# Kernel tuning notes

Hardware: AMD Instinct MI355X
Metric: run time of the kernel (lower is better)

## Reference

```python
import jax, jax.numpy as jnp
import numpy as np

EPS_BN = 1e-5

def _l2n(v, axis):
    return v / jnp.maximum(jnp.linalg.norm(v, axis=axis, keepdims=True), 1e-12)

def _bn_relu(x, g, b):
    # x: [B, C, K]; BatchNorm2d training-mode stats over (B, K) per channel, then ReLU
    m = x.mean(axis=(0, 2), keepdims=True)
    v = x.var(axis=(0, 2), keepdims=True)
    return jax.nn.relu(g[None, :, None] * (x - m) * jax.lax.rsqrt(v + EPS_BN) + b[None, :, None])

def _conv_bn_relu(x, W, g, b):
    # 1x1 conv (no bias) == channel matmul
    return _bn_relu(jnp.einsum('oi,bik->bok', W, x), g, b)

def _graphnet(x, anchor, sigma_p):
    # NetVLAD-style soft assignment; vectorized over clusters (no [B,K,N,C] intermediate)
    B, C, H, W = x.shape
    N = H * W
    sig = jax.nn.sigmoid(sigma_p)                              # [K, C]
    xf = x.reshape(B, C, N).transpose(0, 2, 1)                 # [B, N, C]
    inv_s2 = 1.0 / (sig * sig)                                 # [K, C]
    q = (jnp.einsum('bnc,kc->bnk', xf * xf, inv_s2)
         - 2.0 * jnp.einsum('bnc,kc->bnk', xf, anchor * inv_s2)
         + jnp.sum(anchor * anchor * inv_s2, axis=-1))         # [B, N, K]
    assign = jax.nn.softmax(-0.5 * q.transpose(0, 2, 1), axis=1)  # [B, K, N], softmax over clusters
    s = assign.sum(axis=-1)                                    # [B, K]
    wx = jnp.einsum('bkn,bnc->bkc', assign, xf)                # [B, K, C]
    nodes = (wx - s[..., None] * anchor[None]) / sig[None] / (s[..., None] + 1e-9)
    nodes = _l2n(nodes, 2)
    flat = _l2n(nodes.reshape(B, -1), 1)
    # faithful to torch: flat view as (B, C, K) is a pure reshape of [B, K, C] data
    return flat.reshape(B, C, anchor.shape[0]), assign

def _cascade_gcn(x, W1, W2):
    # loop=2 cascaded GCN: adj = softmax(x^T x), out = (adj @ (x^T W))^T
    for Wg in (W1, W2):
        adj = jax.nn.softmax(jnp.einsum('bik,bil->bkl', x, x), axis=2)   # [B, K, K]
        sup = jnp.einsum('bik,io->bko', x, Wg)                           # [B, K, C]
        x = jnp.einsum('bkl,blo->bok', adj, sup)                         # [B, C, K]
    return jax.nn.relu(x)

def _mutual(edge, r1, r2, assign, g1, g2, cw, cg, cb):
    # cross-graph correlation + cascade GCN + project back to pixels
    a = jax.nn.softmax(jnp.einsum('bik,bil->bkl', edge, r1), axis=-1)    # [B, K, K]
    m = jnp.einsum('bkl,bcl->bck', a, r2)                                # [B, C, K]
    edge = _cascade_gcn(edge + m, g1, g2)
    ex = jnp.einsum('bck,bkn->bcn', edge, assign)                        # [B, C, N]
    return _conv_bn_relu(ex, cw, cg, cb)


def setup_inputs() -> dict:
    key = jax.random.key(0)
    B, C, H, W, K = 16, 256, 64, 64, 8
    ks = jax.random.split(key, 40)
    sc = 1.0 / np.sqrt(C)
    d = {
        'rgb':   jax.random.normal(ks[0], (B, C, H, W), jnp.float32),
        't':     jax.random.normal(ks[1], (B, C, H, W), jnp.float32),
        'edger': jax.random.normal(ks[2], (B, C, H, W), jnp.float32),
        'edget': jax.random.normal(ks[3], (B, C, H, W), jnp.float32),
        'pred_w': jax.random.normal(ks[4], (1, C), jnp.float32) * sc,
        'pred_b': jax.random.normal(ks[5], (1,), jnp.float32) * 0.1,
        'rgb_anchor': jax.random.uniform(ks[6], (K, C), jnp.float32),
        'rgb_sigma':  jax.random.uniform(ks[7], (K, C), jnp.float32),
        't_anchor':   jax.random.uniform(ks[8], (K, C), jnp.float32),
        't_sigma':    jax.random.uniform(ks[9], (K, C), jnp.float32),
    }
    i = 10
    for name in ['rgb_c1', 'rgb_c2', 't_c1', 't_c2', 't2r_conv', 'r2t_conv']:
        d[name + '_w'] = jax.random.normal(ks[i], (C, C), jnp.float32) * sc; i += 1
        d[name + '_g'] = jax.random.uniform(ks[i], (C,), jnp.float32); i += 1
        d[name + '_b'] = jnp.zeros((C,), jnp.float32)
    for name in ['t2r_g1', 't2r_g2', 'r2t_g1', 'r2t_g2']:
        d[name + '_w'] = jax.random.normal(ks[i], (C, C), jnp.float32) * sc; i += 1
    return d


def reference(rgb, t, edger, edget, pred_w, pred_b,
              rgb_anchor, rgb_sigma, t_anchor, t_sigma,
              rgb_c1_w, rgb_c1_g, rgb_c1_b, rgb_c2_w, rgb_c2_g, rgb_c2_b,
              t_c1_w, t_c1_g, t_c1_b, t_c2_w, t_c2_g, t_c2_b,
              t2r_conv_w, t2r_conv_g, t2r_conv_b,
              r2t_conv_w, r2t_conv_g, r2t_conv_b,
              t2r_g1_w, t2r_g2_w, r2t_g1_w, r2t_g2_w):
    # edge-gated features
    edge_r = jnp.einsum('oi,bihw->bohw', pred_w, edger) + pred_b.reshape(1, -1, 1, 1)
    rgb_x = jax.nn.sigmoid(edge_r) * rgb
    edge_t = jnp.einsum('oi,bihw->bohw', pred_w, edget) + pred_b.reshape(1, -1, 1, 1)
    t_x = jax.nn.sigmoid(edge_t) * t
    # graph projection
    rgb_graph, rgb_assign = _graphnet(rgb_x, rgb_anchor, rgb_sigma)
    t_graph, t_assign = _graphnet(t_x, t_anchor, t_sigma)
    rgb_g1 = _conv_bn_relu(rgb_graph, rgb_c1_w, rgb_c1_g, rgb_c1_b)
    rgb_g2 = _conv_bn_relu(rgb_graph, rgb_c2_w, rgb_c2_g, rgb_c2_b)
    t_g1 = _conv_bn_relu(t_graph, t_c1_w, t_c1_g, t_c1_b)
    t_g2 = _conv_bn_relu(t_graph, t_c2_w, t_c2_g, t_c2_b)
    # mutual graph interaction
    n_rgb = _mutual(rgb_graph, t_g1, t_g2, rgb_assign, t2r_g1_w, t2r_g2_w,
                    t2r_conv_w, t2r_conv_g, t2r_conv_b)
    rgb_x = rgb_x + n_rgb.reshape(rgb_x.shape)
    n_t = _mutual(t_graph, rgb_g1, rgb_g2, t_assign, r2t_g1_w, r2t_g2_w,
                  r2t_conv_w, r2t_conv_g, r2t_conv_b)
    t_x = t_x + n_t.reshape(t_x.shape)
    return (rgb_x, t_x)
```

## Files before the change

kernel.cpp:

```cpp
#include <hip/hip_runtime.h>
#include <math.h>

#define BB 16
#define CC 256
#define NN 4096
#define KK 8

#define OFF_S      ((size_t)0)
#define OFF_WX     ((size_t)256)
#define OFF_G      ((size_t)65792)
#define OFF_CS     ((size_t)67840)
#define OFF_MS     ((size_t)69888)
#define OFF_CK     ((size_t)70912)
#define ACC_FLOATS ((size_t)70928)
#define OFF_ASSIGN ((size_t)70928)
#define OFF_GRAPH  ((size_t)1119504)
#define OFF_CLP    ((size_t)1185040)
#define OFF_WT     ((size_t)1193232)
#define OFF_Y      ((size_t)1586448)
#define OFF_CE     ((size_t)1717520)
#define WS_FLOATS  ((size_t)1783056)

__global__ __launch_bounds__(256) void k0_prep(
    const float* __restrict__ w0, const float* __restrict__ w1,
    const float* __restrict__ w2, const float* __restrict__ w3,
    const float* __restrict__ w4, const float* __restrict__ w5,
    const float* __restrict__ anch_r, const float* __restrict__ sig_r,
    const float* __restrict__ anch_t, const float* __restrict__ sig_t,
    float* __restrict__ ws)
{
    int bid = blockIdx.x, tid = threadIdx.x;
    if (bid < 1536) {
        int widx = bid >> 8;
        int e = ((bid & 255) << 8) + tid;
        int o = e >> 8, i = e & 255;
        const float* W = widx == 0 ? w0 : widx == 1 ? w1 : widx == 2 ? w2 :
                         widx == 3 ? w3 : widx == 4 ? w4 : w5;
        ws[OFF_WT + (size_t)widx * 65536 + (size_t)i * 256 + o] = W[o * 256 + i];
    } else {
        int pid = ((bid - 1536) << 8) + tid;
        int M = pid >> 11, j = pid & 2047;
        const float* sg = M ? sig_t : sig_r;
        const float* an = M ? anch_t : anch_r;
        float s = 1.f / (1.f + expf(-sg[j]));
        float is2 = 1.f / (s * s);
        float a = an[j];
        float2* c2 = (float2*)(ws + OFF_CLP);
        c2[(size_t)M * 2048 + j] = make_float2(is2, -2.f * a * is2);
        atomicAdd(&ws[OFF_CK + (size_t)M * 8 + (j >> 8)], a * a * is2);
    }
}

__global__ __launch_bounds__(256) void k1_gate_assign(
    const float* __restrict__ rgb, const float* __restrict__ t,
    const float* __restrict__ edger, const float* __restrict__ edget,
    const float* __restrict__ pred_w, const float* __restrict__ pred_b,
    float* __restrict__ out, float* __restrict__ ws)
{
    int tile = blockIdx.x;
    int b    = blockIdx.y;
    int M    = blockIdx.z;
    int tid  = threadIdx.x;
    int tx = tid & 63, ty = tid >> 6;
    int n0 = tile * 64;

    const float* X = M ? t : rgb;
    const float* E = M ? edget : edger;

    __shared__ _Float16 xs[CC][66];
    __shared__ float2 pr_s[2048];
    __shared__ float qp[KK][4][64];
    __shared__ float gatep[4][64];
    __shared__ float gate[64];
    __shared__ float asg[KK][64];
    __shared__ float cks[KK];

    const float2* pr = (const float2*)(ws + OFF_CLP) + (size_t)M * 2048;
    for (int i = tid; i < 2048; i += 256) pr_s[i] = pr[i];
    if (tid < KK) cks[tid] = ws[OFF_CK + (size_t)M * 8 + tid];

    const float* Eb = E + ((size_t)b * CC) * NN + n0 + tx;
    float acc = 0.f;
    for (int c = ty * 64; c < ty * 64 + 64; ++c)
        acc += pred_w[c] * Eb[(size_t)c * NN];
    gatep[ty][tx] = acc;
    __syncthreads();
    if (tid < 64) {
        float g = gatep[0][tx] + gatep[1][tx] + gatep[2][tx] + gatep[3][tx] + pred_b[0];
        gate[tx] = 1.f / (1.f + expf(-g));
    }
    __syncthreads();

    const float* Xb = X + ((size_t)b * CC) * NN + n0 + tx;
    float* Ob = out + (((size_t)M * BB + b) * CC) * NN + n0 + tx;
    float gt = gate[tx];
    float qk[KK];
#pragma unroll
    for (int k = 0; k < KK; ++k) qk[k] = 0.f;
    for (int c = ty * 64; c < ty * 64 + 64; ++c) {
        float x = gt * Xb[(size_t)c * NN];
        Ob[(size_t)c * NN] = x;
        xs[c][tx] = (_Float16)x;
        float xx = x * x;
#pragma unroll
        for (int k = 0; k < KK; ++k) {
            float2 p = pr_s[k * 256 + c];
            qk[k] += xx * p.x + x * p.y;
        }
    }
#pragma unroll
    for (int k = 0; k < KK; ++k) qp[k][ty][tx] = qk[k];
    __syncthreads();

    float* assign_g = ws + OFF_ASSIGN + (((size_t)M * BB + b) * KK) * NN;
    if (tid < 64) {
        float q[KK], mx = -1e30f;
#pragma unroll
        for (int k = 0; k < KK; ++k) {
            q[k] = -0.5f * (qp[k][0][tx] + qp[k][1][tx] + qp[k][2][tx] + qp[k][3][tx] + cks[k]);
            mx = fmaxf(mx, q[k]);
        }
        float sm = 0.f;
#pragma unroll
        for (int k = 0; k < KK; ++k) { q[k] = expf(q[k] - mx); sm += q[k]; }
        float inv = 1.f / sm;
#pragma unroll
        for (int k = 0; k < KK; ++k) {
            float a = q[k] * inv;
            asg[k][tx] = a;
            assign_g[(size_t)k * NN + n0 + tx] = a;
        }
    }
    __syncthreads();

    {
        int c = tid;
        float a0[KK];
#pragma unroll
        for (int k = 0; k < KK; ++k) a0[k] = 0.f;
        for (int j = 0; j < 64; ++j) {
            float xv = (float)xs[c][j];
#pragma unroll
            for (int k = 0; k < KK; ++k) a0[k] += asg[k][j] * xv;
        }
        float* wx_g = ws + OFF_WX + ((size_t)M * BB + b) * KK * CC;
#pragma unroll
        for (int k = 0; k < KK; ++k)
            atomicAdd(&wx_g[k * CC + c], a0[k]);
    }
    if (tid < 64) {
        int k1 = tid >> 3, k2 = tid & 7;
        float g = 0.f;
        for (int j = 0; j < 64; ++j) g += asg[k1][j] * asg[k2][j];
        atomicAdd(&ws[OFF_G + ((size_t)M * BB + b) * 64 + tid], g);
    } else if (tid < 72) {
        int k = tid - 64;
        float sv = 0.f;
        for (int j = 0; j < 64; ++j) sv += asg[k][j];
        atomicAdd(&ws[OFF_S + ((size_t)M * BB + b) * KK + k], sv);
    }
}

__global__ __launch_bounds__(256) void k2_nodes(
    const float* __restrict__ anch_r, const float* __restrict__ sig_r,
    const float* __restrict__ anch_t, const float* __restrict__ sig_t,
    float* __restrict__ ws)
{
    int b = blockIdx.x & 15, M = blockIdx.x >> 4;
    int c = threadIdx.x;
    const float* an = M ? anch_t : anch_r;
    const float* sg = M ? sig_t : sig_r;
    const float* wx = ws + OFF_WX + ((size_t)M * BB + b) * KK * CC;
    const float* sp = ws + OFF_S + ((size_t)M * BB + b) * KK;
    float* gout = ws + OFF_GRAPH + ((size_t)M * BB + b) * 2048;

    __shared__ float nod[KK][CC];
    __shared__ float nrm[KK];
    __shared__ float gp[CC];
    __shared__ float gnrm;

    float node[KK];
#pragma unroll
    for (int k = 0; k < KK; ++k) {
        float s = sp[k];
        float sig = 1.f / (1.f + expf(-sg[k * CC + c]));
        float v = (wx[k * CC + c] - s * an[k * CC + c]) / sig / (s + 1e-9f);
        node[k] = v;
        nod[k][c] = v;
    }
    __syncthreads();
    if (c < KK) {
        float ss = 0.f;
        for (int i = 0; i < CC; ++i) ss += nod[c][i] * nod[c][i];
        nrm[c] = fmaxf(sqrtf(ss), 1e-12f);
    }
    __syncthreads();
    float gs = 0.f;
#pragma unroll
    for (int k = 0; k < KK; ++k) { node[k] /= nrm[k]; gs += node[k] * node[k]; }
    gp[c] = gs;
    __syncthreads();
    if (c == 0) {
        float ss = 0.f;
        for (int i = 0; i < CC; ++i) ss += gp[i];
        gnrm = fmaxf(sqrtf(ss), 1e-12f);
    }
    __syncthreads();
    float inv = 1.f / gnrm;
#pragma unroll
    for (int k = 0; k < KK; ++k)
        gout[k * CC + c] = node[k] * inv;
}

__global__ __launch_bounds__(256) void k3_conv(float* __restrict__ ws)
{
    int conv = blockIdx.x >> 4, b = blockIdx.x & 15;
    int o = threadIdx.x;
    int M = conv >> 1;
    const float* gsrc = ws + OFF_GRAPH + ((size_t)M * BB + b) * 2048;
    const float* wt = ws + OFF_WT + (size_t)conv * 65536;
    __shared__ float gsh[2048];
    for (int i = o; i < 2048; i += 256) gsh[i] = gsrc[i];
    __syncthreads();
    float acc[KK];
#pragma unroll
    for (int k = 0; k < KK; ++k) acc[k] = 0.f;
    for (int i = 0; i < CC; ++i) {
        float w = wt[(size_t)i * 256 + o];
#pragma unroll
        for (int k = 0; k < KK; ++k) acc[k] += w * gsh[i * 8 + k];
    }
    float* y = ws + OFF_Y + ((size_t)conv * BB + b) * 2048;
    float s1 = 0.f, s2 = 0.f;
#pragma unroll
    for (int k = 0; k < KK; ++k) { y[o * 8 + k] = acc[k]; s1 += acc[k]; s2 += acc[k] * acc[k]; }
    atomicAdd(&ws[OFF_CS + (size_t)conv * 512 + o], s1);
    atomicAdd(&ws[OFF_CS + (size_t)conv * 512 + 256 + o], s2);
}

__device__ __forceinline__ void gcn_layer(const float* __restrict__ Wg,
                                          float* xin, float* xout, float* am,
                                          float* sup, int o, bool do_relu)
{
    if (o < 64) {
        int k = o >> 3, l = o & 7;
        float s = 0.f;
        for (int i = 0; i < CC; ++i) s += xin[i * 9 + k] * xin[i * 9 + l];
        am[k * 9 + l] = s;
    }
    __syncthreads();
    if (o < 8) {
        float mx = -1e30f;
#pragma unroll
        for (int l = 0; l < 8; ++l) mx = fmaxf(mx, am[o * 9 + l]);
        float e[8], sm = 0.f;
#pragma unroll
        for (int l = 0; l < 8; ++l) { e[l] = expf(am[o * 9 + l] - mx); sm += e[l]; }
        float inv = 1.f / sm;
#pragma unroll
        for (int l = 0; l < 8; ++l) am[o * 9 + l] = e[l] * inv;
    }
    float sa[8];
#pragma unroll
    for (int k = 0; k < 8; ++k) sa[k] = 0.f;
    for (int i = 0; i < CC; ++i) {
        float w = Wg[(size_t)i * 256 + o];
#pragma unroll
        for (int k = 0; k < 8; ++k) sa[k] += xin[i * 9 + k] * w;
    }
#pragma unroll
    for (int k = 0; k < 8; ++k) sup[k * 256 + o] = sa[k];
    __syncthreads();
#pragma unroll
    for (int k = 0; k < 8; ++k) {
        float v = 0.f;
#pragma unroll
        for (int l = 0; l < 8; ++l) v += am[k * 9 + l] * sup[l * 256 + o];
        xout[o * 9 + k] = do_relu ? fmaxf(v, 0.f) : v;
    }
    __syncthreads();
}

__global__ __launch_bounds__(256) void k4_mutual(
    const float* __restrict__ rc1g, const float* __restrict__ rc1b,
    const float* __restrict__ rc2g, const float* __restrict__ rc2b,
    const float* __restrict__ tc1g, const float* __restrict__ tc1b,
    const float* __restrict__ tc2g, const float* __restrict__ tc2b,
    const float* __restrict__ t2rg1, const float* __restrict__ t2rg2,
    const float* __restrict__ r2tg1, const float* __restrict__ r2tg2,
    float* __restrict__ ws)
{
    int D = blockIdx.x >> 4, b = blockIdx.x & 15;
    int o = threadIdx.x;
    int M = D;
    int convR1 = D ? 0 : 2;
    int convR2 = D ? 1 : 3;
    const float* g1p = D ? rc1g : tc1g;  const float* b1p = D ? rc1b : tc1b;
    const float* g2p = D ? rc2g : tc2g;  const float* b2p = D ? rc2b : tc2b;
    const float* gcn1 = D ? r2tg1 : t2rg1;
    const float* gcn2 = D ? r2tg2 : t2rg2;
    const float* cwT = ws + OFF_WT + (size_t)(4 + D) * 65536;

    __shared__ float edge_s[CC * 9];
    __shared__ float r1_s[CC * 9];
    __shared__ float r2_s[CC * 9];
    __shared__ float x0[CC * 9];
    __shared__ float x1[CC * 9];
    __shared__ float sup[KK * CC];
    __shared__ float am[KK * 9];
    __shared__ float sS[KK];
    __shared__ float gS[64];

    if (o < 8)  sS[o] = ws[OFF_S + ((size_t)M * BB + b) * 8 + o];
    if (o < 64) gS[o] = ws[OFF_G + ((size_t)M * BB + b) * 64 + o];

    const float* egr = ws + OFF_GRAPH + ((size_t)M * BB + b) * 2048;
    const float* y1 = ws + OFF_Y + ((size_t)convR1 * BB + b) * 2048;
    const float* y2 = ws + OFF_Y + ((size_t)convR2 * BB + b) * 2048;
    float m1 = ws[OFF_CS + (size_t)convR1 * 512 + o] * (1.f / 128.f);
    float q1 = ws[OFF_CS + (size_t)convR1 * 512 + 256 + o] * (1.f / 128.f);
    float al1 = g1p[o] * rsqrtf(q1 - m1 * m1 + 1e-5f);
    float be1 = b1p[o] - m1 * al1;
    float m2 = ws[OFF_CS + (size_t)convR2 * 512 + o] * (1.f / 128.f);
    float q2 = ws[OFF_CS + (size_t)convR2 * 512 + 256 + o] * (1.f / 128.f);
    float al2 = g2p[o] * rsqrtf(q2 - m2 * m2 + 1e-5f);
    float be2 = b2p[o] - m2 * al2;
#pragma unroll
    for (int k = 0; k < 8; ++k) {
        edge_s[o * 9 + k] = egr[o * 8 + k];
        r1_s[o * 9 + k] = fmaxf(al1 * y1[o * 8 + k] + be1, 0.f);
        r2_s[o * 9 + k] = fmaxf(al2 * y2[o * 8 + k] + be2, 0.f);
    }
    __syncthreads();

    if (o < 64) {
        int k = o >> 3, l = o & 7;
        float s = 0.f;
        for (int i = 0; i < CC; ++i) s += edge_s[i * 9 + k] * r1_s[i * 9 + l];
        am[k * 9 + l] = s;
    }
    __syncthreads();
    if (o < 8) {
        float mx = -1e30f;
#pragma unroll
        for (int l = 0; l < 8; ++l) mx = fmaxf(mx, am[o * 9 + l]);
        float e[8], sm = 0.f;
#pragma unroll
        for (int l = 0; l < 8; ++l) { e[l] = expf(am[o * 9 + l] - mx); sm += e[l]; }
        float inv = 1.f / sm;
#pragma unroll
        for (int l = 0; l < 8; ++l) am[o * 9 + l] = e[l] * inv;
    }
    __syncthreads();

#pragma unroll
    for (int k = 0; k < 8; ++k) {
        float mm = 0.f;
#pragma unroll
        for (int l = 0; l < 8; ++l) mm += am[k * 9 + l] * r2_s[o * 9 + l];
        x0[o * 9 + k] = edge_s[o * 9 + k] + mm;
    }
    __syncthreads();

    gcn_layer(gcn1, x0, x1, am, sup, o, false);
    gcn_layer(gcn2, x1, x0, am, sup, o, true);

    float ac[8];
#pragma unroll
    for (int k = 0; k < 8; ++k) ac[k] = 0.f;
    for (int i = 0; i < CC; ++i) {
        float w = cwT[(size_t)i * 256 + o];
#pragma unroll
        for (int k = 0; k < 8; ++k) ac[k] += w * x0[i * 9 + k];
    }
    float* ce = ws + OFF_CE + ((size_t)D * BB + b) * 2048;
    float smv = 0.f, sqv = 0.f;
#pragma unroll
    for (int k = 0; k < 8; ++k) {
        ce[o * 8 + k] = ac[k];
        smv += ac[k] * sS[k];
#pragma unroll
        for (int l = 0; l < 8; ++l) sqv += ac[k] * ac[l] * gS[k * 8 + l];
    }
    atomicAdd(&ws[OFF_MS + (size_t)D * 512 + o], smv);
    atomicAdd(&ws[OFF_MS + (size_t)D * 512 + 256 + o], sqv);
}

__global__ __launch_bounds__(256) void k6_final(
    const float* __restrict__ t2rg, const float* __restrict__ t2rb,
    const float* __restrict__ r2tg, const float* __restrict__ r2tb,
    float* __restrict__ out, const float* __restrict__ ws)
{
    int chunk = blockIdx.x >> 2, cq = blockIdx.x & 3;
    int b = blockIdx.y, D = blockIdx.z;
    int tid = threadIdx.x;
    int n = chunk * 256 + tid;

    const float* assign_g = ws + OFF_ASSIGN + (((size_t)D * BB + b) * KK) * NN;
    float areg[KK];
#pragma unroll
    for (int k = 0; k < KK; ++k) areg[k] = assign_g[(size_t)k * NN + n];

    __shared__ float ce_s[64 * 8];
    __shared__ float al_s[64], be_s[64];
    const float* ce = ws + OFF_CE + ((size_t)D * BB + b) * 2048 + (size_t)cq * 512;
    for (int i = tid; i < 512; i += 256) ce_s[i] = ce[i];
    if (tid < 64) {
        int o = cq * 64 + tid;
        float m = ws[OFF_MS + (size_t)D * 512 + o] * (1.f / 65536.f);
        float q = ws[OFF_MS + (size_t)D * 512 + 256 + o] * (1.f / 65536.f);
        float var = q - m * m;
        const float* g = D ? r2tg : t2rg;
        const float* bb = D ? r2tb : t2rb;
        float al = g[o] * rsqrtf(var + 1e-5f);
        al_s[tid] = al;
        be_s[tid] = bb[o] - m * al;
    }
    __syncthreads();

    float* ob = out + (((size_t)D * BB + b) * CC + (size_t)cq * 64) * NN + n;
    for (int cc = 0; cc < 64; ++cc) {
        float y = 0.f;
#pragma unroll
        for (int k = 0; k < KK; ++k) y += ce_s[cc * 8 + k] * areg[k];
        float v = fmaxf(al_s[cc] * y + be_s[cc], 0.f);
        ob[(size_t)cc * NN] += v;
    }
}

extern "C" void kernel_launch(void* const* d_in, const int* in_sizes, int n_in,
                              void* d_out, int out_size, void* d_ws, size_t ws_size,
                              hipStream_t stream) {
    (void)in_sizes; (void)n_in; (void)out_size; (void)ws_size;
    const float* rgb    = (const float*)d_in[0];
    const float* t      = (const float*)d_in[1];
    const float* edger  = (const float*)d_in[2];
    const float* edget  = (const float*)d_in[3];
    const float* pred_w = (const float*)d_in[4];
    const float* pred_b = (const float*)d_in[5];
    const float* anch_r = (const float*)d_in[6];
    const float* sig_r  = (const float*)d_in[7];
    const float* anch_t = (const float*)d_in[8];
    const float* sig_t  = (const float*)d_in[9];
    const float* rc1w = (const float*)d_in[10];
    const float* rc1g = (const float*)d_in[11];
    const float* rc1b = (const float*)d_in[12];
    const float* rc2w = (const float*)d_in[13];
    const float* rc2g = (const float*)d_in[14];
    const float* rc2b = (const float*)d_in[15];
    const float* tc1w = (const float*)d_in[16];
    const float* tc1g = (const float*)d_in[17];
    const float* tc1b = (const float*)d_in[18];
    const float* tc2w = (const float*)d_in[19];
    const float* tc2g = (const float*)d_in[20];
    const float* tc2b = (const float*)d_in[21];
    const float* t2rcw = (const float*)d_in[22];
    const float* t2rcg = (const float*)d_in[23];
    const float* t2rcb = (const float*)d_in[24];
    const float* r2tcw = (const float*)d_in[25];
    const float* r2tcg = (const float*)d_in[26];
    const float* r2tcb = (const float*)d_in[27];
    const float* t2rg1 = (const float*)d_in[28];
    const float* t2rg2 = (const float*)d_in[29];
    const float* r2tg1 = (const float*)d_in[30];
    const float* r2tg2 = (const float*)d_in[31];

    float* out = (float*)d_out;
    float* ws = (float*)d_ws;

    hipMemsetAsync(ws, 0, ACC_FLOATS * sizeof(float), stream);
    k0_prep<<<1552, 256, 0, stream>>>(rc1w, rc2w, tc1w, tc2w, t2rcw, r2tcw,
                                      anch_r, sig_r, anch_t, sig_t, ws);
    k1_gate_assign<<<dim3(64, 16, 2), 256, 0, stream>>>(rgb, t, edger, edget,
                                                        pred_w, pred_b, out, ws);
    k2_nodes<<<32, 256, 0, stream>>>(anch_r, sig_r, anch_t, sig_t, ws);
    k3_conv<<<64, 256, 0, stream>>>(ws);
    k4_mutual<<<32, 256, 0, stream>>>(rc1g, rc1b, rc2g, rc2b, tc1g, tc1b, tc2g, tc2b,
                                      t2rg1, t2rg2, r2tg1, r2tg2, ws);
    k6_final<<<dim3(64, 16, 2), 256, 0, stream>>>(t2rcg, t2rcb, r2tcg, r2tcb, out, ws);
}
```

Before: 594.5 us.

## Recompute gated features in final kernel instead of writing then re-reading output

The gate-assign kernel no longer writes the full gated feature map to the output. It stores only the per-pixel gate value in channel 0 of the output slot. The final kernel reads that gate and the original input, recomputes gate*x and adds the graph term in a single write, removing one full-tensor write and one read-modify-write pass. The prep kernel's cluster parameters are re-laid out as [c][k] so they can be read with float4 global loads instead of being staged in shared memory, and the final kernel uses 512-thread blocks covering all 256 channels. The cost is re-reading the input tensor in the final kernel.

```diff
diff --git a/kernel.cpp b/kernel.cpp
--- a/kernel.cpp
+++ b/kernel.cpp
@@ -40,14 +40,15 @@
     } else {
         int pid = ((bid - 1536) << 8) + tid;
         int M = pid >> 11, j = pid & 2047;
+        int k = j >> 8, c = j & 255;
         const float* sg = M ? sig_t : sig_r;
         const float* an = M ? anch_t : anch_r;
         float s = 1.f / (1.f + expf(-sg[j]));
         float is2 = 1.f / (s * s);
         float a = an[j];
         float2* c2 = (float2*)(ws + OFF_CLP);
-        c2[(size_t)M * 2048 + j] = make_float2(is2, -2.f * a * is2);
-        atomicAdd(&ws[OFF_CK + (size_t)M * 8 + (j >> 8)], a * a * is2);
+        c2[(size_t)M * 2048 + (size_t)c * 8 + k] = make_float2(is2, -2.f * a * is2);
+        atomicAdd(&ws[OFF_CK + (size_t)M * 8 + k], a * a * is2);
     }
 }
 
@@ -68,45 +69,48 @@
     const float* E = M ? edget : edger;
 
     __shared__ _Float16 xs[CC][66];
-    __shared__ float2 pr_s[2048];
     __shared__ float qp[KK][4][64];
     __shared__ float gatep[4][64];
-    __shared__ float gate[64];
+    __shared__ float gate_s[64];
     __shared__ float asg[KK][64];
     __shared__ float cks[KK];
 
-    const float2* pr = (const float2*)(ws + OFF_CLP) + (size_t)M * 2048;
-    for (int i = tid; i < 2048; i += 256) pr_s[i] = pr[i];
     if (tid < KK) cks[tid] = ws[OFF_CK + (size_t)M * 8 + tid];
 
     const float* Eb = E + ((size_t)b * CC) * NN + n0 + tx;
     float acc = 0.f;
+#pragma unroll 4
     for (int c = ty * 64; c < ty * 64 + 64; ++c)
         acc += pred_w[c] * Eb[(size_t)c * NN];
     gatep[ty][tx] = acc;
     __syncthreads();
     if (tid < 64) {
         float g = gatep[0][tx] + gatep[1][tx] + gatep[2][tx] + gatep[3][tx] + pred_b[0];
-        gate[tx] = 1.f / (1.f + expf(-g));
+        float sg = 1.f / (1.f + expf(-g));
+        gate_s[tx] = sg;
+        out[(((size_t)M * BB + b) * CC) * NN + n0 + tx] = sg;
     }
     __syncthreads();
 
     const float* Xb = X + ((size_t)b * CC) * NN + n0 + tx;
-    float* Ob = out + (((size_t)M * BB + b) * CC) * NN + n0 + tx;
-    float gt = gate[tx];
+    const float4* prq = (const float4*)(ws + OFF_CLP) + (size_t)M * 1024;
+    float gt = gate_s[tx];
     float qk[KK];
 #pragma unroll
     for (int k = 0; k < KK; ++k) qk[k] = 0.f;
+#pragma unroll 2
     for (int c = ty * 64; c < ty * 64 + 64; ++c) {
         float x = gt * Xb[(size_t)c * NN];
-        Ob[(size_t)c * NN] = x;
         xs[c][tx] = (_Float16)x;
         float xx = x * x;
-#pragma unroll
-        for (int k = 0; k < KK; ++k) {
-            float2 p = pr_s[k * 256 + c];
-            qk[k] += xx * p.x + x * p.y;
-        }
+        float4 p0 = prq[c * 4 + 0];
+        float4 p1 = prq[c * 4 + 1];
+        float4 p2 = prq[c * 4 + 2];
+        float4 p3 = prq[c * 4 + 3];
+        qk[0] += xx * p0.x + x * p0.y;  qk[1] += xx * p0.z + x * p0.w;
+        qk[2] += xx * p1.x + x * p1.y;  qk[3] += xx * p1.z + x * p1.w;
+        qk[4] += xx * p2.x + x * p2.y;  qk[5] += xx * p2.z + x * p2.w;
+        qk[6] += xx * p3.x + x * p3.y;  qk[7] += xx * p3.z + x * p3.w;
     }
 #pragma unroll
     for (int k = 0; k < KK; ++k) qp[k][ty][tx] = qk[k];
@@ -138,6 +142,7 @@
         float a0[KK];
 #pragma unroll
         for (int k = 0; k < KK; ++k) a0[k] = 0.f;
+#pragma unroll 4
         for (int j = 0; j < 64; ++j) {
             float xv = (float)xs[c][j];
 #pragma unroll
@@ -386,45 +391,56 @@
     atomicAdd(&ws[OFF_MS + (size_t)D * 512 + 256 + o], sqv);
 }
 
-__global__ __launch_bounds__(256) void k6_final(
+__global__ __launch_bounds__(512) void k6_final(
+    const float* __restrict__ rgb, const float* __restrict__ t,
     const float* __restrict__ t2rg, const float* __restrict__ t2rb,
     const float* __restrict__ r2tg, const float* __restrict__ r2tb,
     float* __restrict__ out, const float* __restrict__ ws)
 {
-    int chunk = blockIdx.x >> 2, cq = blockIdx.x & 3;
+    int chunk = blockIdx.x;
     int b = blockIdx.y, D = blockIdx.z;
     int tid = threadIdx.x;
-    int n = chunk * 256 + tid;
+    int tn = tid & 255, th = tid >> 8;
+    int n = chunk * 256 + tn;
+
+    const float* X = D ? t : rgb;
+    float* obase = out + (((size_t)D * BB + b) * CC) * NN;
+
+    float gt = obase[n];
 
     const float* assign_g = ws + OFF_ASSIGN + (((size_t)D * BB + b) * KK) * NN;
-    float areg[KK];
-#pragma unroll
-    for (int k = 0; k < KK; ++k) areg[k] = assign_g[(size_t)k * NN + n];
-
-    __shared__ float ce_s[64 * 8];
-    __shared__ float al_s[64], be_s[64];
-    const float* ce = ws + OFF_CE + ((size_t)D * BB + b) * 2048 + (size_t)cq * 512;
-    for (int i = tid; i < 512; i += 256) ce_s[i] = ce[i];
-    if (tid < 64) {
-        int o = cq * 64 + tid;
+    float a0 = assign_g[0 * NN + n], a1 = assign_g[1 * NN + n];
+    float a2 = assign_g[2 * NN + n], a3 = assign_g[3 * NN + n];
+    float a4 = assign_g[4 * NN + n], a5 = assign_g[5 * NN + n];
+    float a6 = assign_g[6 * NN + n], a7 = assign_g[7 * NN + n];
+
+    __shared__ __align__(16) float ce_s[2048];
+    __shared__ float al_s[256], be_s[256];
+    const float* ce = ws + OFF_CE + ((size_t)D * BB + b) * 2048;
+    for (int i = tid; i < 2048; i += 512) ce_s[i] = ce[i];
+    if (tid < 256) {
+        int o = tid;
         float m = ws[OFF_MS + (size_t)D * 512 + o] * (1.f / 65536.f);
         float q = ws[OFF_MS + (size_t)D * 512 + 256 + o] * (1.f / 65536.f);
-        float var = q - m * m;
         const float* g = D ? r2tg : t2rg;
         const float* bb = D ? r2tb : t2rb;
-        float al = g[o] * rsqrtf(var + 1e-5f);
-        al_s[tid] = al;
-        be_s[tid] = bb[o] - m * al;
-    }
-    __syncthreads();
-
-    float* ob = out + (((size_t)D * BB + b) * CC + (size_t)cq * 64) * NN + n;
-    for (int cc = 0; cc < 64; ++cc) {
-        float y = 0.f;
-#pragma unroll
-        for (int k = 0; k < KK; ++k) y += ce_s[cc * 8 + k] * areg[k];
-        float v = fmaxf(al_s[cc] * y + be_s[cc], 0.f);
-        ob[(size_t)cc * NN] += v;
+        float al = g[o] * rsqrtf(q - m * m + 1e-5f);
+        al_s[o] = al;
+        be_s[o] = bb[o] - m * al;
+    }
+    __syncthreads();
+
+    const float* Xb = X + ((size_t)b * CC) * NN + n;
+    const float4* ce4 = (const float4*)ce_s;
+#pragma unroll 4
+    for (int i = 0; i < 128; ++i) {
+        int c = th * 128 + i;
+        float4 ca = ce4[2 * c];
+        float4 cb = ce4[2 * c + 1];
+        float y = ca.x * a0 + ca.y * a1 + ca.z * a2 + ca.w * a3
+                + cb.x * a4 + cb.y * a5 + cb.z * a6 + cb.w * a7;
+        float v = fmaxf(al_s[c] * y + be_s[c], 0.f);
+        obase[(size_t)c * NN + n] = gt * Xb[(size_t)c * NN] + v;
     }
 }
 
@@ -477,5 +493,6 @@
     k3_conv<<<64, 256, 0, stream>>>(ws);
     k4_mutual<<<32, 256, 0, stream>>>(rc1g, rc1b, rc2g, rc2b, tc1g, tc1b, tc2g, tc2b,
                                       t2rg1, t2rg2, r2tg1, r2tg2, ws);
-    k6_final<<<dim3(64, 16, 2), 256, 0, stream>>>(t2rcg, t2rcb, r2tcg, r2tcb, out, ws);
-}
+    k6_final<<<dim3(16, 16, 2), 512, 0, stream>>>(rgb, t, t2rcg, t2rcb, r2tcg, r2tcb,
+                                                  out, ws);
+}
```

Measured after the change: 626.8 us. 5.4% more time.
